# Kernel tuning notes

Measured on AMD Instinct MI355X. Metric: run time of the kernel, lower is better.

## Reference

```python
import jax, jax.numpy as jnp
import numpy as np

N_ENT = 40000      # n_ent_vocab
NUM_POS = 24       # n_rel_vocab // 2
N_REL = 48         # n_rel_vocab (fwd + inverse relations)
BODY_LEN = 3
N_EDGES = 300000
BATCH = 64
THR = 1e-20


def setup_inputs() -> dict:
    key = jax.random.key(0)
    ks = jax.random.split(key, 8)
    return {
        "q_head": jax.random.randint(ks[0], (BATCH,), 0, N_ENT, dtype=jnp.int32),
        "q_rel": jax.random.randint(ks[1], (BATCH,), 0, NUM_POS, dtype=jnp.int32),
        "t": jax.random.randint(ks[2], (BATCH,), 0, N_ENT, dtype=jnp.int32),
        # dec_output is a softmax over relations -> positive weights in (0,1)
        "attention": jax.random.uniform(ks[3], (BATCH, BODY_LEN, N_REL), dtype=jnp.float32),
        "edge_head": jax.random.randint(ks[4], (N_EDGES,), 0, N_ENT, dtype=jnp.int32),
        "edge_tail": jax.random.randint(ks[5], (N_EDGES,), 0, N_ENT, dtype=jnp.int32),
        "edge_rel": jax.random.randint(ks[6], (N_EDGES,), 0, NUM_POS, dtype=jnp.int32),
        # uncertain-KG confidence values stored in the sparse adjacency
        "edge_val": jax.random.uniform(ks[7], (N_EDGES,), dtype=jnp.float32),
    }


def reference(q_head, q_rel, t, attention, edge_head, edge_tail, edge_rel, edge_val):
    """Fused equivalent of Translator.forwardAllNLP.

    database[r] are sparse [N_ENT, N_ENT] matrices; here the whole multigraph is
    one edge list (edge_head, edge_tail, edge_rel, edge_val). torch.sparse.mm
    per relation + attention-weighted accumulation becomes a single gather /
    segment_sum pass over all relations at once.
    """
    B = q_head.shape[0]
    # zero out the query triples in the (shared) database, as in the torch code
    killed = ((edge_head[None, :] == q_head[:, None])
              & (edge_tail[None, :] == t[:, None])
              & (edge_rel[None, :] == q_rel[:, None])).any(axis=0)
    vals = jnp.where(killed, 0.0, edge_val)  # [E]

    mem = jax.nn.one_hot(q_head, N_ENT, dtype=jnp.float32)  # [B, N_ENT]
    for step in range(BODY_LEN):
        attn = attention[:, step]                 # [B, N_REL]
        a_fwd = attn[:, edge_rel]                 # [B, E]  attention[:,step,r]
        a_rev = attn[:, edge_rel + NUM_POS]       # [B, E]  attention[:,step,r+num_pos]
        gh = mem[:, edge_head] * vals             # [B, E]  sparse.mm(mem, A_r)
        gt = mem[:, edge_tail] * vals             # [B, E]  sparse.mm(mem, A_r^T)
        fwd_msg = jax.ops.segment_sum((gh * a_fwd).T, edge_tail, num_segments=N_ENT).T
        rev_msg = jax.ops.segment_sum((gt * a_rev).T, edge_head, num_segments=N_ENT).T
        # self-loop term: memories * attention[:, step, -1]
        mem = fwd_msg + rev_msg + mem * attn[:, -1:]

    mem = mem / jnp.maximum(THR, mem.sum(axis=1, keepdims=True))
    # -sum(one_hot(t) * log(max(thr, mem))) == -log(max(thr, mem[b, t[b]]))
    tgt_prob = mem[jnp.arange(B), t]
    batch_loss = -jnp.log(jnp.maximum(THR, tgt_prob)).mean()
    return batch_loss, mem
```

## Files before the change

### kernel.cpp

```cpp
#include <hip/hip_runtime.h>

#define N_ENT 40000
#define NB 64
#define BODY_LEN 3
#define N_REL 48
#define NUM_POS 24
#define THR 1e-20f

#define NBK 157
#define PA_BLOCKS 320
#define DEC_BLOCKS 320
#define FLIST_LDS 192


__global__ void k_zero(int* __restrict__ bktCnt, int* __restrict__ fcnt,
                       float* __restrict__ sums) {
    int t = threadIdx.x;
    if (t < NBK) bktCnt[t] = 0;
    if (t < 3) fcnt[t] = 0;
    if (t < NB) sums[t] = 0.0f;
}

__global__ void k_bhist(const int* __restrict__ eh, const int* __restrict__ et,
                        int* __restrict__ bktCnt, int nE) {
    __shared__ int h[NBK];
    int tid = threadIdx.x;
    for (int i = tid; i < NBK; i += 256) h[i] = 0;
    __syncthreads();
    for (int i = blockIdx.x * 256 + tid; i < nE; i += gridDim.x * 256) {
        atomicAdd(&h[eh[i] >> 8], 1);
        atomicAdd(&h[et[i] >> 8], 1);
    }
    __syncthreads();
    for (int i = tid; i < NBK; i += 256)
        if (h[i]) atomicAdd(&bktCnt[i], h[i]);
}

__global__ void k_bscan(const int* __restrict__ bktCnt, int* __restrict__ bktBase,
                        int* __restrict__ bktCur, int* __restrict__ offs) {
    __shared__ int s[256];
    int t = threadIdx.x;
    int v = (t < NBK) ? bktCnt[t] : 0;
    s[t] = v;
    __syncthreads();
    for (int off = 1; off < 256; off <<= 1) {
        int add = (t >= off) ? s[t - off] : 0;
        __syncthreads();
        s[t] += add;
        __syncthreads();
    }
    if (t < NBK) {
        int ex = s[t] - v;
        bktBase[t] = ex;
        bktCur[t] = ex;
    }
    if (t == NBK - 1) {
        bktBase[NBK] = s[t];
        offs[N_ENT] = s[t];
    }
}

__global__ void k_passA(const int* __restrict__ qh, const int* __restrict__ qr,
                        const int* __restrict__ tq, const int* __restrict__ eh,
                        const int* __restrict__ et, const int* __restrict__ er,
                        const float* __restrict__ ev, int* __restrict__ bktCur,
                        uint2* __restrict__ items, int nE) {
    __shared__ long long s_key[NB];
    __shared__ int h[NBK];
    __shared__ int myB[NBK];
    int tid = threadIdx.x;
    if (tid < NB)
        s_key[tid] = ((long long)qh[tid] << 32) | ((long long)tq[tid] << 8) | (long long)qr[tid];
    for (int i = tid; i < NBK; i += 256) h[i] = 0;
    __syncthreads();
    int chunk = (nE + PA_BLOCKS - 1) / PA_BLOCKS;
    int b0 = blockIdx.x * chunk;
    int b1 = min(nE, b0 + chunk);
    for (int i = b0 + tid; i < b1; i += 256) {
        atomicAdd(&h[eh[i] >> 8], 1);
        atomicAdd(&h[et[i] >> 8], 1);
    }
    __syncthreads();
    for (int i = tid; i < NBK; i += 256) {
        int c = h[i];
        myB[i] = c ? atomicAdd(&bktCur[i], c) : 0;
        h[i] = 0;
    }
    __syncthreads();
    for (int i = b0 + tid; i < b1; i += 256) {
        int hh = eh[i], te = et[i], r = er[i];
        long long k = ((long long)hh << 32) | ((long long)te << 8) | (long long)r;
        bool killed = false;
#pragma unroll
        for (int b = 0; b < NB; ++b) killed |= (s_key[b] == k);
        unsigned vb = killed ? 0u : __float_as_uint(ev[i]);
        int bk1 = hh >> 8;
        int rk1 = atomicAdd(&h[bk1], 1);
        items[myB[bk1] + rk1] =
            make_uint2((unsigned)te | ((unsigned)r << 16) | ((unsigned)(hh & 255) << 24), vb);
        int bk2 = te >> 8;
        int rk2 = atomicAdd(&h[bk2], 1);
        items[myB[bk2] + rk2] =
            make_uint2((unsigned)hh | ((unsigned)(r + NUM_POS) << 16) | ((unsigned)(te & 255) << 24), vb);
    }
}

__global__ void k_passB(const uint2* __restrict__ itemsA, const int* __restrict__ bktBase,
                        int* __restrict__ offs, uint2* __restrict__ csr) {
    __shared__ int cnt[256];
    __shared__ int sc[256];
    int tid = threadIdx.x;
    int b = blockIdx.x;
    int e0 = b << 8;
    int eCnt = min(256, N_ENT - e0);
    cnt[tid] = 0;
    __syncthreads();
    int ib = bktBase[b];
    int n = bktBase[b + 1] - ib;
    for (int i = tid; i < n; i += 256)
        atomicAdd(&cnt[itemsA[ib + i].x >> 24], 1);
    __syncthreads();
    int v = cnt[tid];
    sc[tid] = v;
    __syncthreads();
    for (int off = 1; off < 256; off <<= 1) {
        int add = (tid >= off) ? sc[tid - off] : 0;
        __syncthreads();
        sc[tid] += add;
        __syncthreads();
    }
    int ex = sc[tid] - v;
    if (tid < eCnt) offs[e0 + tid] = ib + ex;
    cnt[tid] = ex;
    __syncthreads();
    for (int i = tid; i < n; i += 256) {
        uint2 it = itemsA[ib + i];
        int k = (int)(it.x >> 24);
        int p = atomicAdd(&cnt[k], 1);
        csr[ib + p] = it;
    }
}

__device__ __forceinline__ void flag_entities(unsigned long long m, int lane,
                                              int ent, int* s_cnt, int* s_list) {
    bool flag = ((lane & 15) == 0) && ((m >> lane) & 0xFFFFULL);
    unsigned long long am = __ballot(flag);
    if (am) {
        int leader = __ffsll((long long)am) - 1;
        int lb = 0;
        if (lane == leader) lb = atomicAdd(s_cnt, __popcll(am));
        lb = __shfl(lb, leader);
        if (flag) {
            int rank = __popcll(am & ((1ULL << lane) - 1ULL));
            s_list[lb + rank] = ent;
        }
    }
}

__global__ void k_init_decay(const int* __restrict__ qh, const float* __restrict__ attn,
                             float* __restrict__ nxt, int* __restrict__ fcnt,
                             int* __restrict__ flist) {
    __shared__ float s_d[NB];
    __shared__ int s_q[NB];
    __shared__ int s_list[FLIST_LDS];
    __shared__ int s_cnt, s_gbase;
    int tid = threadIdx.x;
    if (tid < NB) {
        s_d[tid] = attn[tid * (BODY_LEN * N_REL) + 0 * N_REL + (N_REL - 1)];
        s_q[tid] = qh[tid];
    }
    if (tid == 0) s_cnt = 0;
    __syncthreads();
    int lane = tid & 63;
    const int total4 = NB * N_ENT / 4;
    for (int i4 = blockIdx.x * 256 + tid; i4 < total4; i4 += gridDim.x * 256) {
        int ent = (i4 * 4) >> 6;
        int b0 = (i4 * 4) & 63;
        float4 w;
        w.x = (s_q[b0 + 0] == ent) ? s_d[b0 + 0] : 0.0f;
        w.y = (s_q[b0 + 1] == ent) ? s_d[b0 + 1] : 0.0f;
        w.z = (s_q[b0 + 2] == ent) ? s_d[b0 + 2] : 0.0f;
        w.w = (s_q[b0 + 3] == ent) ? s_d[b0 + 3] : 0.0f;
        ((float4*)nxt)[i4] = w;
        bool nz = (s_q[b0 + 0] == ent) | (s_q[b0 + 1] == ent) |
                  (s_q[b0 + 2] == ent) | (s_q[b0 + 3] == ent);
        unsigned long long m = __ballot(nz);
        flag_entities(m, lane, ent, &s_cnt, s_list);
    }
    __syncthreads();
    if (tid == 0 && s_cnt) s_gbase = atomicAdd(fcnt, s_cnt);
    __syncthreads();
    for (int i = tid; i < s_cnt; i += 256) flist[s_gbase + i] = s_list[i];
}

__global__ void k_decay(const float* __restrict__ oldm, float* __restrict__ nxt,
                        const float* __restrict__ attn, int step,
                        int* __restrict__ fcnt, int* __restrict__ flist) {
    __shared__ float s_d[NB];
    __shared__ int s_list[FLIST_LDS];
    __shared__ int s_cnt, s_gbase;
    int tid = threadIdx.x;
    if (tid < NB)
        s_d[tid] = attn[tid * (BODY_LEN * N_REL) + step * N_REL + (N_REL - 1)];
    if (tid == 0) s_cnt = 0;
    __syncthreads();
    int lane = tid & 63;
    const int total4 = NB * N_ENT / 4;
    for (int i4 = blockIdx.x * 256 + tid; i4 < total4; i4 += gridDim.x * 256) {
        float4 v = ((const float4*)oldm)[i4];
        int b0 = (tid * 4) & 63;
        float4 w;
        w.x = v.x * s_d[b0 + 0];
        w.y = v.y * s_d[b0 + 1];
        w.z = v.z * s_d[b0 + 2];
        w.w = v.w * s_d[b0 + 3];
        ((float4*)nxt)[i4] = w;
        bool nz = (v.x != 0.0f) | (v.y != 0.0f) | (v.z != 0.0f) | (v.w != 0.0f);
        unsigned long long m = __ballot(nz);
        flag_entities(m, lane, (i4 * 4) >> 6, &s_cnt, s_list);
    }
    __syncthreads();
    if (tid == 0 && s_cnt) s_gbase = atomicAdd(fcnt, s_cnt);
    __syncthreads();
    for (int i = tid; i < s_cnt; i += 256) flist[s_gbase + i] = s_list[i];
}

template <bool STEP0>
__global__ __launch_bounds__(256) void k_fstep(
    const uint2* __restrict__ csr, const int* __restrict__ offs,
    const int* __restrict__ flist, const int* __restrict__ fcnt,
    const float* __restrict__ attn, int step,
    const float* __restrict__ oldm, const int* __restrict__ qh,
    float* __restrict__ nxt) {
    __shared__ float s_attn[NB][N_REL + 1];
    int tid = threadIdx.x;
    for (int idx = tid; idx < NB * N_REL; idx += 256) {
        int b = idx / N_REL, r = idx % N_REL;
        s_attn[b][r] = attn[b * (BODY_LEN * N_REL) + step * N_REL + r];
    }
    __syncthreads();
    int lane = tid & 63;
    int myqh = STEP0 ? qh[lane] : 0;
    int n = *fcnt;
    int w = (blockIdx.x * 256 + tid) >> 6;
    int nW = (gridDim.x * 256) >> 6;
    for (int f = w; f < n; f += nW) {
        int e = flist[f];
        float src = STEP0 ? ((myqh == e) ? 1.0f : 0.0f)
                          : oldm[(size_t)e * 64 + lane];
        int base = offs[e];
        int cnt = offs[e + 1] - base;
        for (int k0 = 0; k0 < cnt; k0 += 64) {
            uint2 slot = make_uint2(0u, 0u);
            if (k0 + lane < cnt) slot = csr[base + k0 + lane];
            int lim = min(64, cnt - k0);
            for (int j = 0; j < lim; ++j) {
                unsigned meta = (unsigned)__shfl((int)slot.x, j);
                float v = __uint_as_float((unsigned)__shfl((int)slot.y, j));
                if (v == 0.0f) continue;
                float val = src * v * s_attn[lane][(meta >> 16) & 63];
                if (val != 0.0f)
                    atomicAdd(&nxt[(size_t)(meta & 0xFFFFu) * 64 + lane], val);
            }
        }
    }
}

__global__ void k_sums(const float* __restrict__ mem, float* __restrict__ sums) {
    __shared__ float s_s[NB];
    if (threadIdx.x < NB) s_s[threadIdx.x] = 0.0f;
    __syncthreads();
    const float4* m4 = (const float4*)mem;
    const int total4 = NB * N_ENT / 4;
    float4 acc = {0.0f, 0.0f, 0.0f, 0.0f};
    for (int i = blockIdx.x * 256 + threadIdx.x; i < total4; i += gridDim.x * 256) {
        float4 v = m4[i];
        acc.x += v.x; acc.y += v.y; acc.z += v.z; acc.w += v.w;
    }
    int b0 = (threadIdx.x * 4) & 63;
    atomicAdd(&s_s[b0 + 0], acc.x);
    atomicAdd(&s_s[b0 + 1], acc.y);
    atomicAdd(&s_s[b0 + 2], acc.z);
    atomicAdd(&s_s[b0 + 3], acc.w);
    __syncthreads();
    if (threadIdx.x < NB) atomicAdd(&sums[threadIdx.x], s_s[threadIdx.x]);
}

__global__ void k_norm_tr(const float* __restrict__ mem, const float* __restrict__ sums,
                          const int* __restrict__ tt, float* __restrict__ out) {
    if (blockIdx.x == N_ENT / 64) {
        int b = threadIdx.x;
        if (b < 64) {
            float p = mem[(size_t)tt[b] * 64 + b] / fmaxf(THR, sums[b]);
            float l = -logf(fmaxf(THR, p));
#pragma unroll
            for (int off = 32; off > 0; off >>= 1) l += __shfl_down(l, off);
            if (b == 0) out[0] = l * (1.0f / 64.0f);
        }
        return;
    }
    __shared__ float tile[64][65];
    __shared__ float s_inv[64];
    int tid = threadIdx.x;
    int e0 = blockIdx.x * 64;
    if (tid < 64) s_inv[tid] = 1.0f / fmaxf(THR, sums[tid]);
    const float4* m4 = (const float4*)(mem + (size_t)e0 * 64);
#pragma unroll
    for (int k = 0; k < 4; ++k) {
        int i4 = k * 256 + tid;
        float4 v = m4[i4];
        int el = i4 >> 4, b0 = (i4 * 4) & 63;
        tile[el][b0 + 0] = v.x; tile[el][b0 + 1] = v.y;
        tile[el][b0 + 2] = v.z; tile[el][b0 + 3] = v.w;
    }
    __syncthreads();
#pragma unroll
    for (int k = 0; k < 16; ++k) {
        int idx = k * 256 + tid;
        int el = idx & 63, b = idx >> 6;
        out[1 + (size_t)b * N_ENT + e0 + el] = tile[el][b] * s_inv[b];
    }
}

extern "C" void kernel_launch(void* const* d_in, const int* in_sizes, int n_in,
                              void* d_out, int out_size, void* d_ws, size_t ws_size,
                              hipStream_t stream) {
    const int*   qh   = (const int*)d_in[0];
    const int*   qr   = (const int*)d_in[1];
    const int*   tt   = (const int*)d_in[2];
    const float* attn = (const float*)d_in[3];
    const int*   eh   = (const int*)d_in[4];
    const int*   et   = (const int*)d_in[5];
    const int*   er   = (const int*)d_in[6];
    const float* ev   = (const float*)d_in[7];
    float* out = (float*)d_out;
    int nE = in_sizes[4];

    const size_t MEM_BYTES = (size_t)NB * N_ENT * sizeof(float);
    char* ws = (char*)d_ws;
    int*   offs    = (int*)ws;
    int*   flist   = (int*)(ws + (192u << 10));
    int*   bktCnt  = (int*)(ws + (384u << 10));
    int*   bktBase = (int*)(ws + (388u << 10));
    int*   bktCur  = (int*)(ws + (392u << 10));
    int*   fcnt    = (int*)(ws + (396u << 10));
    float* sums    = (float*)(ws + (400u << 10));
    uint2* csr     = (uint2*)(ws + (1u << 20));
    float* memA    = (float*)(ws + (6u << 20));
    float* memB;
    uint2* itemsA;
    size_t itemsBytes = (size_t)2 * nE * sizeof(uint2);
    size_t needBoth = (size_t)(6u << 20) + 2 * MEM_BYTES + itemsBytes;
    if (ws_size >= needBoth) {
        memB   = (float*)(ws + (6u << 20) + MEM_BYTES);
        itemsA = (uint2*)(ws + (6u << 20) + 2 * MEM_BYTES);
    } else {
        memB   = out + 1;
        itemsA = (uint2*)(out + 1);
    }

    k_zero<<<1, 256, 0, stream>>>(bktCnt, fcnt, sums);
    k_bhist<<<PA_BLOCKS, 256, 0, stream>>>(eh, et, bktCnt, nE);
    k_bscan<<<1, 256, 0, stream>>>(bktCnt, bktBase, bktCur, offs);
    k_passA<<<PA_BLOCKS, 256, 0, stream>>>(qh, qr, tt, eh, et, er, ev, bktCur, itemsA, nE);
    k_passB<<<NBK, 256, 0, stream>>>(itemsA, bktBase, offs, csr);

    k_init_decay<<<DEC_BLOCKS, 256, 0, stream>>>(qh, attn, memA, fcnt + 0, flist);
    k_fstep<true><<<16, 256, 0, stream>>>(csr, offs, flist, fcnt + 0, attn, 0,
                                          nullptr, qh, memA);
    float* curm = memA;
    float* nxtm = memB;
    for (int s = 1; s < BODY_LEN; ++s) {
        k_decay<<<DEC_BLOCKS, 256, 0, stream>>>(curm, nxtm, attn, s, fcnt + s, flist);
        k_fstep<false><<<1024, 256, 0, stream>>>(csr, offs, flist, fcnt + s, attn, s,
                                                 curm, nullptr, nxtm);
        float* tmp = curm; curm = nxtm; nxtm = tmp;
    }

    k_sums<<<128, 256, 0, stream>>>(curm, sums);
    k_norm_tr<<<N_ENT / 64 + 1, 256, 0, stream>>>(curm, sums, tt, out);
}
```

Before: 200.1 us.

## Switch propagation to pull-based gather with per-entity activity flags

```diff
diff --git a/kernel.cpp b/kernel.cpp
--- a/kernel.cpp
+++ b/kernel.cpp
@@ -9,39 +9,36 @@
 
 #define NBK 157
 #define PA_BLOCKS 320
-#define DEC_BLOCKS 320
-#define FLIST_LDS 192
-
-
-__global__ void k_zero(int* __restrict__ bktCnt, int* __restrict__ fcnt,
-                       float* __restrict__ sums) {
-    int t = threadIdx.x;
-    if (t < NBK) bktCnt[t] = 0;
-    if (t < 3) fcnt[t] = 0;
-    if (t < NB) sums[t] = 0.0f;
-}
-
-__global__ void k_bhist(const int* __restrict__ eh, const int* __restrict__ et,
-                        int* __restrict__ bktCnt, int nE) {
+#define STEP_BLOCKS 2048
+
+
+__global__ void k_hist(const int* __restrict__ eh, const int* __restrict__ et,
+                       int* __restrict__ pHist, int nE) {
     __shared__ int h[NBK];
     int tid = threadIdx.x;
     for (int i = tid; i < NBK; i += 256) h[i] = 0;
     __syncthreads();
-    for (int i = blockIdx.x * 256 + tid; i < nE; i += gridDim.x * 256) {
+    int chunk = (nE + PA_BLOCKS - 1) / PA_BLOCKS;
+    int b0 = blockIdx.x * chunk, b1 = min(nE, b0 + chunk);
+    for (int i = b0 + tid; i < b1; i += 256) {
+        atomicAdd(&h[et[i] >> 8], 1);
         atomicAdd(&h[eh[i] >> 8], 1);
-        atomicAdd(&h[et[i] >> 8], 1);
-    }
-    __syncthreads();
-    for (int i = tid; i < NBK; i += 256)
-        if (h[i]) atomicAdd(&bktCnt[i], h[i]);
-}
-
-__global__ void k_bscan(const int* __restrict__ bktCnt, int* __restrict__ bktBase,
-                        int* __restrict__ bktCur, int* __restrict__ offs) {
+    }
+    __syncthreads();
+    for (int i = tid; i < NBK; i += 256) pHist[blockIdx.x * NBK + i] = h[i];
+}
+
+__global__ void k_bscan(int* __restrict__ pHist, int* __restrict__ bktBase,
+                        int* __restrict__ offs, const int* __restrict__ qh,
+                        unsigned char* __restrict__ act0, float* __restrict__ sums) {
     __shared__ int s[256];
     int t = threadIdx.x;
-    int v = (t < NBK) ? bktCnt[t] : 0;
-    s[t] = v;
+    int tot = 0;
+    if (t < NBK) {
+#pragma unroll 8
+        for (int i = 0; i < PA_BLOCKS; ++i) tot += pHist[i * NBK + t];
+    }
+    s[t] = tot;
     __syncthreads();
     for (int off = 1; off < 256; off <<= 1) {
         int add = (t >= off) ? s[t - off] : 0;
@@ -49,44 +46,38 @@
         s[t] += add;
         __syncthreads();
     }
+    int ex = s[t] - tot;
+    if (t < NBK) bktBase[t] = ex;
+    if (t == NBK - 1) { bktBase[NBK] = s[t]; offs[N_ENT] = s[t]; }
     if (t < NBK) {
-        int ex = s[t] - v;
-        bktBase[t] = ex;
-        bktCur[t] = ex;
-    }
-    if (t == NBK - 1) {
-        bktBase[NBK] = s[t];
-        offs[N_ENT] = s[t];
-    }
+        int run = ex;
+#pragma unroll 4
+        for (int i = 0; i < PA_BLOCKS; ++i) {
+            int c = pHist[i * NBK + t];
+            pHist[i * NBK + t] = run;
+            run += c;
+        }
+    }
+    for (int i = t; i < N_ENT; i += 256) act0[i] = 0;
+    for (int i = t; i < NB * 16; i += 256) sums[i] = 0.0f;
+    __syncthreads();
+    if (t < NB) act0[qh[t]] = 1;
 }
 
 __global__ void k_passA(const int* __restrict__ qh, const int* __restrict__ qr,
                         const int* __restrict__ tq, const int* __restrict__ eh,
                         const int* __restrict__ et, const int* __restrict__ er,
-                        const float* __restrict__ ev, int* __restrict__ bktCur,
+                        const float* __restrict__ ev, const int* __restrict__ pBase,
                         uint2* __restrict__ items, int nE) {
     __shared__ long long s_key[NB];
-    __shared__ int h[NBK];
-    __shared__ int myB[NBK];
+    __shared__ int cur[NBK];
     int tid = threadIdx.x;
     if (tid < NB)
         s_key[tid] = ((long long)qh[tid] << 32) | ((long long)tq[tid] << 8) | (long long)qr[tid];
-    for (int i = tid; i < NBK; i += 256) h[i] = 0;
+    for (int i = tid; i < NBK; i += 256) cur[i] = pBase[blockIdx.x * NBK + i];
     __syncthreads();
     int chunk = (nE + PA_BLOCKS - 1) / PA_BLOCKS;
-    int b0 = blockIdx.x * chunk;
-    int b1 = min(nE, b0 + chunk);
-    for (int i = b0 + tid; i < b1; i += 256) {
-        atomicAdd(&h[eh[i] >> 8], 1);
-        atomicAdd(&h[et[i] >> 8], 1);
-    }
-    __syncthreads();
-    for (int i = tid; i < NBK; i += 256) {
-        int c = h[i];
-        myB[i] = c ? atomicAdd(&bktCur[i], c) : 0;
-        h[i] = 0;
-    }
-    __syncthreads();
+    int b0 = blockIdx.x * chunk, b1 = min(nE, b0 + chunk);
     for (int i = b0 + tid; i < b1; i += 256) {
         int hh = eh[i], te = et[i], r = er[i];
         long long k = ((long long)hh << 32) | ((long long)te << 8) | (long long)r;
@@ -94,14 +85,14 @@
 #pragma unroll
         for (int b = 0; b < NB; ++b) killed |= (s_key[b] == k);
         unsigned vb = killed ? 0u : __float_as_uint(ev[i]);
-        int bk1 = hh >> 8;
-        int rk1 = atomicAdd(&h[bk1], 1);
-        items[myB[bk1] + rk1] =
-            make_uint2((unsigned)te | ((unsigned)r << 16) | ((unsigned)(hh & 255) << 24), vb);
-        int bk2 = te >> 8;
-        int rk2 = atomicAdd(&h[bk2], 1);
-        items[myB[bk2] + rk2] =
-            make_uint2((unsigned)hh | ((unsigned)(r + NUM_POS) << 16) | ((unsigned)(te & 255) << 24), vb);
+        int bk = te >> 8;
+        int p = atomicAdd(&cur[bk], 1);
+        items[p] = make_uint2((unsigned)hh | ((unsigned)r << 16) |
+                              ((unsigned)(te & 255) << 24), vb);
+        bk = hh >> 8;
+        p = atomicAdd(&cur[bk], 1);
+        items[p] = make_uint2((unsigned)te | ((unsigned)(r + NUM_POS) << 16) |
+                              ((unsigned)(hh & 255) << 24), vb);
     }
 }
 
@@ -141,149 +132,68 @@
     }
 }
 
-__device__ __forceinline__ void flag_entities(unsigned long long m, int lane,
-                                              int ent, int* s_cnt, int* s_list) {
-    bool flag = ((lane & 15) == 0) && ((m >> lane) & 0xFFFFULL);
-    unsigned long long am = __ballot(flag);
-    if (am) {
-        int leader = __ffsll((long long)am) - 1;
-        int lb = 0;
-        if (lane == leader) lb = atomicAdd(s_cnt, __popcll(am));
-        lb = __shfl(lb, leader);
-        if (flag) {
-            int rank = __popcll(am & ((1ULL << lane) - 1ULL));
-            s_list[lb + rank] = ent;
-        }
-    }
-}
-
-__global__ void k_init_decay(const int* __restrict__ qh, const float* __restrict__ attn,
-                             float* __restrict__ nxt, int* __restrict__ fcnt,
-                             int* __restrict__ flist) {
-    __shared__ float s_d[NB];
+template <int STEP>
+__global__ __launch_bounds__(256) void k_step(
+    const uint2* __restrict__ csr, const int* __restrict__ offs,
+    const unsigned char* __restrict__ actIn, unsigned char* __restrict__ actOut,
+    const float* __restrict__ attn, const float* __restrict__ oldm,
+    const int* __restrict__ qh, float* __restrict__ nxt, float* __restrict__ sums) {
+    __shared__ float s_attn[NB][N_REL + 1];
+    __shared__ float s_dlast[NB];
     __shared__ int s_q[NB];
-    __shared__ int s_list[FLIST_LDS];
-    __shared__ int s_cnt, s_gbase;
-    int tid = threadIdx.x;
-    if (tid < NB) {
-        s_d[tid] = attn[tid * (BODY_LEN * N_REL) + 0 * N_REL + (N_REL - 1)];
-        s_q[tid] = qh[tid];
-    }
-    if (tid == 0) s_cnt = 0;
-    __syncthreads();
-    int lane = tid & 63;
-    const int total4 = NB * N_ENT / 4;
-    for (int i4 = blockIdx.x * 256 + tid; i4 < total4; i4 += gridDim.x * 256) {
-        int ent = (i4 * 4) >> 6;
-        int b0 = (i4 * 4) & 63;
-        float4 w;
-        w.x = (s_q[b0 + 0] == ent) ? s_d[b0 + 0] : 0.0f;
-        w.y = (s_q[b0 + 1] == ent) ? s_d[b0 + 1] : 0.0f;
-        w.z = (s_q[b0 + 2] == ent) ? s_d[b0 + 2] : 0.0f;
-        w.w = (s_q[b0 + 3] == ent) ? s_d[b0 + 3] : 0.0f;
-        ((float4*)nxt)[i4] = w;
-        bool nz = (s_q[b0 + 0] == ent) | (s_q[b0 + 1] == ent) |
-                  (s_q[b0 + 2] == ent) | (s_q[b0 + 3] == ent);
-        unsigned long long m = __ballot(nz);
-        flag_entities(m, lane, ent, &s_cnt, s_list);
-    }
-    __syncthreads();
-    if (tid == 0 && s_cnt) s_gbase = atomicAdd(fcnt, s_cnt);
-    __syncthreads();
-    for (int i = tid; i < s_cnt; i += 256) flist[s_gbase + i] = s_list[i];
-}
-
-__global__ void k_decay(const float* __restrict__ oldm, float* __restrict__ nxt,
-                        const float* __restrict__ attn, int step,
-                        int* __restrict__ fcnt, int* __restrict__ flist) {
-    __shared__ float s_d[NB];
-    __shared__ int s_list[FLIST_LDS];
-    __shared__ int s_cnt, s_gbase;
-    int tid = threadIdx.x;
-    if (tid < NB)
-        s_d[tid] = attn[tid * (BODY_LEN * N_REL) + step * N_REL + (N_REL - 1)];
-    if (tid == 0) s_cnt = 0;
-    __syncthreads();
-    int lane = tid & 63;
-    const int total4 = NB * N_ENT / 4;
-    for (int i4 = blockIdx.x * 256 + tid; i4 < total4; i4 += gridDim.x * 256) {
-        float4 v = ((const float4*)oldm)[i4];
-        int b0 = (tid * 4) & 63;
-        float4 w;
-        w.x = v.x * s_d[b0 + 0];
-        w.y = v.y * s_d[b0 + 1];
-        w.z = v.z * s_d[b0 + 2];
-        w.w = v.w * s_d[b0 + 3];
-        ((float4*)nxt)[i4] = w;
-        bool nz = (v.x != 0.0f) | (v.y != 0.0f) | (v.z != 0.0f) | (v.w != 0.0f);
-        unsigned long long m = __ballot(nz);
-        flag_entities(m, lane, (i4 * 4) >> 6, &s_cnt, s_list);
-    }
-    __syncthreads();
-    if (tid == 0 && s_cnt) s_gbase = atomicAdd(fcnt, s_cnt);
-    __syncthreads();
-    for (int i = tid; i < s_cnt; i += 256) flist[s_gbase + i] = s_list[i];
-}
-
-template <bool STEP0>
-__global__ __launch_bounds__(256) void k_fstep(
-    const uint2* __restrict__ csr, const int* __restrict__ offs,
-    const int* __restrict__ flist, const int* __restrict__ fcnt,
-    const float* __restrict__ attn, int step,
-    const float* __restrict__ oldm, const int* __restrict__ qh,
-    float* __restrict__ nxt) {
-    __shared__ float s_attn[NB][N_REL + 1];
-    int tid = threadIdx.x;
+    __shared__ float s_s[NB];
+    int tid = threadIdx.x, lane = tid & 63;
     for (int idx = tid; idx < NB * N_REL; idx += 256) {
         int b = idx / N_REL, r = idx % N_REL;
-        s_attn[b][r] = attn[b * (BODY_LEN * N_REL) + step * N_REL + r];
-    }
-    __syncthreads();
-    int lane = tid & 63;
-    int myqh = STEP0 ? qh[lane] : 0;
-    int n = *fcnt;
+        s_attn[b][r] = attn[b * (BODY_LEN * N_REL) + STEP * N_REL + r];
+    }
+    if (tid < NB) {
+        s_dlast[tid] = attn[tid * (BODY_LEN * N_REL) + STEP * N_REL + (N_REL - 1)];
+        if (STEP == 0) s_q[tid] = qh[tid];
+        if (STEP == 2) s_s[tid] = 0.0f;
+    }
+    __syncthreads();
+    int myq = (STEP == 0) ? s_q[lane] : 0;
+    float colsum = 0.0f;
     int w = (blockIdx.x * 256 + tid) >> 6;
     int nW = (gridDim.x * 256) >> 6;
-    for (int f = w; f < n; f += nW) {
-        int e = flist[f];
-        float src = STEP0 ? ((myqh == e) ? 1.0f : 0.0f)
-                          : oldm[(size_t)e * 64 + lane];
-        int base = offs[e];
-        int cnt = offs[e + 1] - base;
+    for (int d = w; d < N_ENT; d += nW) {
+        float acc = 0.0f;
+        if (STEP == 0) {
+            acc = (myq == d) ? s_dlast[lane] : 0.0f;
+        } else {
+            if (actIn[d]) acc = oldm[(size_t)d * 64 + lane] * s_dlast[lane];
+        }
+        int base = offs[d];
+        int cnt = offs[d + 1] - base;
         for (int k0 = 0; k0 < cnt; k0 += 64) {
-            uint2 slot = make_uint2(0u, 0u);
-            if (k0 + lane < cnt) slot = csr[base + k0 + lane];
-            int lim = min(64, cnt - k0);
-            for (int j = 0; j < lim; ++j) {
-                unsigned meta = (unsigned)__shfl((int)slot.x, j);
-                float v = __uint_as_float((unsigned)__shfl((int)slot.y, j));
-                if (v == 0.0f) continue;
-                float val = src * v * s_attn[lane][(meta >> 16) & 63];
-                if (val != 0.0f)
-                    atomicAdd(&nxt[(size_t)(meta & 0xFFFFu) * 64 + lane], val);
+            int i = k0 + lane;
+            uint2 it = (i < cnt) ? csr[base + i] : make_uint2(0u, 0u);
+            bool on = (i < cnt) && (it.y != 0u) && actIn[it.x & 0xFFFFu];
+            unsigned long long m = __ballot(on);
+            while (m) {
+                int j = __ffsll((long long)m) - 1;
+                m &= m - 1;
+                unsigned mx = (unsigned)__shfl((int)it.x, j);
+                float v = __uint_as_float((unsigned)__shfl((int)it.y, j));
+                int s2 = (int)(mx & 0xFFFFu);
+                float sv = (STEP == 0) ? ((myq == s2) ? 1.0f : 0.0f)
+                                       : oldm[(size_t)s2 * 64 + lane];
+                acc += sv * v * s_attn[lane][(mx >> 16) & 63];
             }
         }
-    }
-}
-
-__global__ void k_sums(const float* __restrict__ mem, float* __restrict__ sums) {
-    __shared__ float s_s[NB];
-    if (threadIdx.x < NB) s_s[threadIdx.x] = 0.0f;
-    __syncthreads();
-    const float4* m4 = (const float4*)mem;
-    const int total4 = NB * N_ENT / 4;
-    float4 acc = {0.0f, 0.0f, 0.0f, 0.0f};
-    for (int i = blockIdx.x * 256 + threadIdx.x; i < total4; i += gridDim.x * 256) {
-        float4 v = m4[i];
-        acc.x += v.x; acc.y += v.y; acc.z += v.z; acc.w += v.w;
-    }
-    int b0 = (threadIdx.x * 4) & 63;
-    atomicAdd(&s_s[b0 + 0], acc.x);
-    atomicAdd(&s_s[b0 + 1], acc.y);
-    atomicAdd(&s_s[b0 + 2], acc.z);
-    atomicAdd(&s_s[b0 + 3], acc.w);
-    __syncthreads();
-    if (threadIdx.x < NB) atomicAdd(&sums[threadIdx.x], s_s[threadIdx.x]);
+        nxt[(size_t)d * 64 + lane] = acc;
+        if (STEP < 2) {
+            unsigned long long nz = __ballot(acc != 0.0f);
+            if (lane == 0) actOut[d] = nz ? 1 : 0;
+        }
+        if (STEP == 2) colsum += acc;
+    }
+    if (STEP == 2) {
+        atomicAdd(&s_s[lane], colsum);
+        __syncthreads();
+        if (tid < NB) atomicAdd(&sums[tid * 16], s_s[tid]);
+    }
 }
 
 __global__ void k_norm_tr(const float* __restrict__ mem, const float* __restrict__ sums,
@@ -291,7 +201,7 @@
     if (blockIdx.x == N_ENT / 64) {
         int b = threadIdx.x;
         if (b < 64) {
-            float p = mem[(size_t)tt[b] * 64 + b] / fmaxf(THR, sums[b]);
+            float p = mem[(size_t)tt[b] * 64 + b] / fmaxf(THR, sums[b * 16]);
             float l = -logf(fmaxf(THR, p));
 #pragma unroll
             for (int off = 32; off > 0; off >>= 1) l += __shfl_down(l, off);
@@ -303,7 +213,7 @@
     __shared__ float s_inv[64];
     int tid = threadIdx.x;
     int e0 = blockIdx.x * 64;
-    if (tid < 64) s_inv[tid] = 1.0f / fmaxf(THR, sums[tid]);
+    if (tid < 64) s_inv[tid] = 1.0f / fmaxf(THR, sums[tid * 16]);
     const float4* m4 = (const float4*)(mem + (size_t)e0 * 64);
 #pragma unroll
     for (int k = 0; k < 4; ++k) {
@@ -339,12 +249,11 @@
     const size_t MEM_BYTES = (size_t)NB * N_ENT * sizeof(float);
     char* ws = (char*)d_ws;
     int*   offs    = (int*)ws;
-    int*   flist   = (int*)(ws + (192u << 10));
-    int*   bktCnt  = (int*)(ws + (384u << 10));
-    int*   bktBase = (int*)(ws + (388u << 10));
-    int*   bktCur  = (int*)(ws + (392u << 10));
-    int*   fcnt    = (int*)(ws + (396u << 10));
-    float* sums    = (float*)(ws + (400u << 10));
+    int*   bktBase = (int*)(ws + (192u << 10));
+    int*   pHist   = (int*)(ws + (196u << 10));
+    unsigned char* act0 = (unsigned char*)(ws + (452u << 10));
+    unsigned char* act1 = (unsigned char*)(ws + (512u << 10));
+    float* sums    = (float*)(ws + (576u << 10));
     uint2* csr     = (uint2*)(ws + (1u << 20));
     float* memA    = (float*)(ws + (6u << 20));
     float* memB;
@@ -359,24 +268,17 @@
         itemsA = (uint2*)(out + 1);
     }
 
-    k_zero<<<1, 256, 0, stream>>>(bktCnt, fcnt, sums);
-    k_bhist<<<PA_BLOCKS, 256, 0, stream>>>(eh, et, bktCnt, nE);
-    k_bscan<<<1, 256, 0, stream>>>(bktCnt, bktBase, bktCur, offs);
-    k_passA<<<PA_BLOCKS, 256, 0, stream>>>(qh, qr, tt, eh, et, er, ev, bktCur, itemsA, nE);
+    k_hist<<<PA_BLOCKS, 256, 0, stream>>>(eh, et, pHist, nE);
+    k_bscan<<<1, 256, 0, stream>>>(pHist, bktBase, offs, qh, act0, sums);
+    k_passA<<<PA_BLOCKS, 256, 0, stream>>>(qh, qr, tt, eh, et, er, ev, pHist, itemsA, nE);
     k_passB<<<NBK, 256, 0, stream>>>(itemsA, bktBase, offs, csr);
 
-    k_init_decay<<<DEC_BLOCKS, 256, 0, stream>>>(qh, attn, memA, fcnt + 0, flist);
-    k_fstep<true><<<16, 256, 0, stream>>>(csr, offs, flist, fcnt + 0, attn, 0,
-                                          nullptr, qh, memA);
-    float* curm = memA;
-    float* nxtm = memB;
-    for (int s = 1; s < BODY_LEN; ++s) {
-        k_decay<<<DEC_BLOCKS, 256, 0, stream>>>(curm, nxtm, attn, s, fcnt + s, flist);
-        k_fstep<false><<<1024, 256, 0, stream>>>(csr, offs, flist, fcnt + s, attn, s,
-                                                 curm, nullptr, nxtm);
-        float* tmp = curm; curm = nxtm; nxtm = tmp;
-    }
-
-    k_sums<<<128, 256, 0, stream>>>(curm, sums);
-    k_norm_tr<<<N_ENT / 64 + 1, 256, 0, stream>>>(curm, sums, tt, out);
-}
+    k_step<0><<<STEP_BLOCKS, 256, 0, stream>>>(csr, offs, act0, act1, attn,
+                                               nullptr, qh, memA, nullptr);
+    k_step<1><<<STEP_BLOCKS, 256, 0, stream>>>(csr, offs, act1, act0, attn,
+                                               memA, qh, memB, nullptr);
+    k_step<2><<<STEP_BLOCKS, 256, 0, stream>>>(csr, offs, act0, nullptr, attn,
+                                               memB, qh, memA, sums);
+
+    k_norm_tr<<<N_ENT / 64 + 1, 256, 0, stream>>>(memA, sums, tt, out);
+}
```

Result: slower. 232.2 us (+16.0%).

## Fuse setup kernels, use per-block histogram offsets, fold column sums into final step

Applied to the files above, without the earlier changes.

```diff
diff --git a/kernel.cpp b/kernel.cpp
--- a/kernel.cpp
+++ b/kernel.cpp
@@ -7,86 +7,115 @@
 #define NUM_POS 24
 #define THR 1e-20f
 
-#define NBK 157
+#define NBK 313
 #define PA_BLOCKS 320
 #define DEC_BLOCKS 320
 #define FLIST_LDS 192
 
 
-__global__ void k_zero(int* __restrict__ bktCnt, int* __restrict__ fcnt,
-                       float* __restrict__ sums) {
+__global__ void k_build0(const int* __restrict__ eh, const int* __restrict__ et,
+                         int* __restrict__ pHist, const int* __restrict__ qh,
+                         const float* __restrict__ attn, float* __restrict__ memA,
+                         int* __restrict__ fcnt, int* __restrict__ flist,
+                         float* __restrict__ sums, int nE) {
+    int tid = threadIdx.x;
+    if (blockIdx.x < PA_BLOCKS) {
+        __shared__ int h[NBK];
+        for (int i = tid; i < NBK; i += 256) h[i] = 0;
+        __syncthreads();
+        int chunk = (nE + PA_BLOCKS - 1) / PA_BLOCKS;
+        int b0 = blockIdx.x * chunk, b1 = min(nE, b0 + chunk);
+        for (int i = b0 + tid; i < b1; i += 256) {
+            atomicAdd(&h[eh[i] >> 7], 1);
+            atomicAdd(&h[et[i] >> 7], 1);
+        }
+        __syncthreads();
+        for (int i = tid; i < NBK; i += 256) pHist[blockIdx.x * NBK + i] = h[i];
+    } else {
+        __shared__ float s_d[NB];
+        __shared__ int s_q[NB];
+        if (tid < NB) {
+            s_d[tid] = attn[tid * (BODY_LEN * N_REL) + 0 * N_REL + (N_REL - 1)];
+            s_q[tid] = qh[tid];
+        }
+        __syncthreads();
+        int ib = blockIdx.x - PA_BLOCKS;
+        const int total4 = NB * N_ENT / 4;
+        for (int i4 = ib * 256 + tid; i4 < total4; i4 += 320 * 256) {
+            int ent = (i4 * 4) >> 6;
+            int b0 = (i4 * 4) & 63;
+            float4 w;
+            w.x = (s_q[b0 + 0] == ent) ? s_d[b0 + 0] : 0.0f;
+            w.y = (s_q[b0 + 1] == ent) ? s_d[b0 + 1] : 0.0f;
+            w.z = (s_q[b0 + 2] == ent) ? s_d[b0 + 2] : 0.0f;
+            w.w = (s_q[b0 + 3] == ent) ? s_d[b0 + 3] : 0.0f;
+            ((float4*)memA)[i4] = w;
+        }
+        if (ib == 0) {
+            for (int i = tid; i < NB * 16; i += 256) sums[i] = 0.0f;
+            if (tid < 64) {
+                int q = s_q[tid];
+                bool first = true;
+                for (int j = 0; j < tid; ++j) first &= (s_q[j] != q);
+                unsigned long long mf = __ballot(first);
+                int pos = __popcll(mf & ((1ULL << tid) - 1ULL));
+                if (first) flist[pos] = q;
+                if (tid == 0) fcnt[0] = __popcll(mf);
+                if (tid == 1) fcnt[1] = 0;
+                if (tid == 2) fcnt[2] = 0;
+            }
+        }
+    }
+}
+
+__global__ void k_bcol(int* __restrict__ pHist, int* __restrict__ bktTot) {
+    __shared__ int s[512];
+    int t = threadIdx.x, b = blockIdx.x;
+    int v = (t < PA_BLOCKS) ? pHist[t * NBK + b] : 0;
+    s[t] = v;
+    __syncthreads();
+    for (int off = 1; off < 512; off <<= 1) {
+        int add = (t >= off) ? s[t - off] : 0;
+        __syncthreads();
+        s[t] += add;
+        __syncthreads();
+    }
+    if (t < PA_BLOCKS) pHist[t * NBK + b] = s[t] - v;
+    if (t == PA_BLOCKS - 1) bktTot[b] = s[t];
+}
+
+__global__ void k_bscan_small(const int* __restrict__ bktTot, int* __restrict__ bktBase,
+                              int* __restrict__ offs) {
+    __shared__ int s[512];
     int t = threadIdx.x;
-    if (t < NBK) bktCnt[t] = 0;
-    if (t < 3) fcnt[t] = 0;
-    if (t < NB) sums[t] = 0.0f;
-}
-
-__global__ void k_bhist(const int* __restrict__ eh, const int* __restrict__ et,
-                        int* __restrict__ bktCnt, int nE) {
-    __shared__ int h[NBK];
-    int tid = threadIdx.x;
-    for (int i = tid; i < NBK; i += 256) h[i] = 0;
-    __syncthreads();
-    for (int i = blockIdx.x * 256 + tid; i < nE; i += gridDim.x * 256) {
-        atomicAdd(&h[eh[i] >> 8], 1);
-        atomicAdd(&h[et[i] >> 8], 1);
-    }
-    __syncthreads();
-    for (int i = tid; i < NBK; i += 256)
-        if (h[i]) atomicAdd(&bktCnt[i], h[i]);
-}
-
-__global__ void k_bscan(const int* __restrict__ bktCnt, int* __restrict__ bktBase,
-                        int* __restrict__ bktCur, int* __restrict__ offs) {
-    __shared__ int s[256];
-    int t = threadIdx.x;
-    int v = (t < NBK) ? bktCnt[t] : 0;
+    int v = (t < NBK) ? bktTot[t] : 0;
     s[t] = v;
     __syncthreads();
-    for (int off = 1; off < 256; off <<= 1) {
+    for (int off = 1; off < 512; off <<= 1) {
         int add = (t >= off) ? s[t - off] : 0;
         __syncthreads();
         s[t] += add;
         __syncthreads();
     }
-    if (t < NBK) {
-        int ex = s[t] - v;
-        bktBase[t] = ex;
-        bktCur[t] = ex;
-    }
-    if (t == NBK - 1) {
-        bktBase[NBK] = s[t];
-        offs[N_ENT] = s[t];
-    }
+    if (t < NBK) bktBase[t] = s[t] - v;
+    if (t == NBK - 1) { bktBase[NBK] = s[t]; offs[N_ENT] = s[t]; }
 }
 
 __global__ void k_passA(const int* __restrict__ qh, const int* __restrict__ qr,
                         const int* __restrict__ tq, const int* __restrict__ eh,
                         const int* __restrict__ et, const int* __restrict__ er,
-                        const float* __restrict__ ev, int* __restrict__ bktCur,
-                        uint2* __restrict__ items, int nE) {
+                        const float* __restrict__ ev, const int* __restrict__ pBase,
+                        const int* __restrict__ bktBase, uint2* __restrict__ items, int nE) {
     __shared__ long long s_key[NB];
-    __shared__ int h[NBK];
-    __shared__ int myB[NBK];
+    __shared__ int cur[NBK];
     int tid = threadIdx.x;
     if (tid < NB)
         s_key[tid] = ((long long)qh[tid] << 32) | ((long long)tq[tid] << 8) | (long long)qr[tid];
-    for (int i = tid; i < NBK; i += 256) h[i] = 0;
+    for (int i = tid; i < NBK; i += 256)
+        cur[i] = bktBase[i] + pBase[blockIdx.x * NBK + i];
     __syncthreads();
     int chunk = (nE + PA_BLOCKS - 1) / PA_BLOCKS;
-    int b0 = blockIdx.x * chunk;
-    int b1 = min(nE, b0 + chunk);
-    for (int i = b0 + tid; i < b1; i += 256) {
-        atomicAdd(&h[eh[i] >> 8], 1);
-        atomicAdd(&h[et[i] >> 8], 1);
-    }
-    __syncthreads();
-    for (int i = tid; i < NBK; i += 256) {
-        int c = h[i];
-        myB[i] = c ? atomicAdd(&bktCur[i], c) : 0;
-        h[i] = 0;
-    }
-    __syncthreads();
+    int b0 = blockIdx.x * chunk, b1 = min(nE, b0 + chunk);
     for (int i = b0 + tid; i < b1; i += 256) {
         int hh = eh[i], te = et[i], r = er[i];
         long long k = ((long long)hh << 32) | ((long long)te << 8) | (long long)r;
@@ -94,33 +123,33 @@
 #pragma unroll
         for (int b = 0; b < NB; ++b) killed |= (s_key[b] == k);
         unsigned vb = killed ? 0u : __float_as_uint(ev[i]);
-        int bk1 = hh >> 8;
-        int rk1 = atomicAdd(&h[bk1], 1);
-        items[myB[bk1] + rk1] =
-            make_uint2((unsigned)te | ((unsigned)r << 16) | ((unsigned)(hh & 255) << 24), vb);
-        int bk2 = te >> 8;
-        int rk2 = atomicAdd(&h[bk2], 1);
-        items[myB[bk2] + rk2] =
-            make_uint2((unsigned)hh | ((unsigned)(r + NUM_POS) << 16) | ((unsigned)(te & 255) << 24), vb);
+        int bk = hh >> 7;
+        int p = atomicAdd(&cur[bk], 1);
+        items[p] = make_uint2((unsigned)te | ((unsigned)r << 16) |
+                              ((unsigned)(hh & 127) << 24), vb);
+        bk = te >> 7;
+        p = atomicAdd(&cur[bk], 1);
+        items[p] = make_uint2((unsigned)hh | ((unsigned)(r + NUM_POS) << 16) |
+                              ((unsigned)(te & 127) << 24), vb);
     }
 }
 
 __global__ void k_passB(const uint2* __restrict__ itemsA, const int* __restrict__ bktBase,
                         int* __restrict__ offs, uint2* __restrict__ csr) {
-    __shared__ int cnt[256];
+    __shared__ int cnt[128];
     __shared__ int sc[256];
     int tid = threadIdx.x;
     int b = blockIdx.x;
-    int e0 = b << 8;
-    int eCnt = min(256, N_ENT - e0);
-    cnt[tid] = 0;
+    int e0 = b << 7;
+    int eCnt = min(128, N_ENT - e0);
+    if (tid < 128) cnt[tid] = 0;
     __syncthreads();
     int ib = bktBase[b];
     int n = bktBase[b + 1] - ib;
     for (int i = tid; i < n; i += 256)
         atomicAdd(&cnt[itemsA[ib + i].x >> 24], 1);
     __syncthreads();
-    int v = cnt[tid];
+    int v = (tid < 128) ? cnt[tid] : 0;
     sc[tid] = v;
     __syncthreads();
     for (int off = 1; off < 256; off <<= 1) {
@@ -131,7 +160,7 @@
     }
     int ex = sc[tid] - v;
     if (tid < eCnt) offs[e0 + tid] = ib + ex;
-    cnt[tid] = ex;
+    if (tid < 128) cnt[tid] = ex;
     __syncthreads();
     for (int i = tid; i < n; i += 256) {
         uint2 it = itemsA[ib + i];
@@ -157,64 +186,34 @@
     }
 }
 
-__global__ void k_init_decay(const int* __restrict__ qh, const float* __restrict__ attn,
-                             float* __restrict__ nxt, int* __restrict__ fcnt,
-                             int* __restrict__ flist) {
+__global__ void k_decay(const float* __restrict__ oldm, float* __restrict__ nxt,
+                        const float* __restrict__ attn, int step,
+                        int* __restrict__ fcnt, int* __restrict__ flist,
+                        float* __restrict__ sums) {
     __shared__ float s_d[NB];
-    __shared__ int s_q[NB];
+    __shared__ float s_s[NB];
     __shared__ int s_list[FLIST_LDS];
     __shared__ int s_cnt, s_gbase;
     int tid = threadIdx.x;
     if (tid < NB) {
-        s_d[tid] = attn[tid * (BODY_LEN * N_REL) + 0 * N_REL + (N_REL - 1)];
-        s_q[tid] = qh[tid];
+        s_d[tid] = attn[tid * (BODY_LEN * N_REL) + step * N_REL + (N_REL - 1)];
+        s_s[tid] = 0.0f;
     }
     if (tid == 0) s_cnt = 0;
     __syncthreads();
     int lane = tid & 63;
-    const int total4 = NB * N_ENT / 4;
-    for (int i4 = blockIdx.x * 256 + tid; i4 < total4; i4 += gridDim.x * 256) {
-        int ent = (i4 * 4) >> 6;
-        int b0 = (i4 * 4) & 63;
-        float4 w;
-        w.x = (s_q[b0 + 0] == ent) ? s_d[b0 + 0] : 0.0f;
-        w.y = (s_q[b0 + 1] == ent) ? s_d[b0 + 1] : 0.0f;
-        w.z = (s_q[b0 + 2] == ent) ? s_d[b0 + 2] : 0.0f;
-        w.w = (s_q[b0 + 3] == ent) ? s_d[b0 + 3] : 0.0f;
-        ((float4*)nxt)[i4] = w;
-        bool nz = (s_q[b0 + 0] == ent) | (s_q[b0 + 1] == ent) |
-                  (s_q[b0 + 2] == ent) | (s_q[b0 + 3] == ent);
-        unsigned long long m = __ballot(nz);
-        flag_entities(m, lane, ent, &s_cnt, s_list);
-    }
-    __syncthreads();
-    if (tid == 0 && s_cnt) s_gbase = atomicAdd(fcnt, s_cnt);
-    __syncthreads();
-    for (int i = tid; i < s_cnt; i += 256) flist[s_gbase + i] = s_list[i];
-}
-
-__global__ void k_decay(const float* __restrict__ oldm, float* __restrict__ nxt,
-                        const float* __restrict__ attn, int step,
-                        int* __restrict__ fcnt, int* __restrict__ flist) {
-    __shared__ float s_d[NB];
-    __shared__ int s_list[FLIST_LDS];
-    __shared__ int s_cnt, s_gbase;
-    int tid = threadIdx.x;
-    if (tid < NB)
-        s_d[tid] = attn[tid * (BODY_LEN * N_REL) + step * N_REL + (N_REL - 1)];
-    if (tid == 0) s_cnt = 0;
-    __syncthreads();
-    int lane = tid & 63;
+    int b0 = (tid * 4) & 63;
+    float cs0 = 0.0f, cs1 = 0.0f, cs2 = 0.0f, cs3 = 0.0f;
     const int total4 = NB * N_ENT / 4;
     for (int i4 = blockIdx.x * 256 + tid; i4 < total4; i4 += gridDim.x * 256) {
         float4 v = ((const float4*)oldm)[i4];
-        int b0 = (tid * 4) & 63;
         float4 w;
         w.x = v.x * s_d[b0 + 0];
         w.y = v.y * s_d[b0 + 1];
         w.z = v.z * s_d[b0 + 2];
         w.w = v.w * s_d[b0 + 3];
         ((float4*)nxt)[i4] = w;
+        if (sums) { cs0 += w.x; cs1 += w.y; cs2 += w.z; cs3 += w.w; }
         bool nz = (v.x != 0.0f) | (v.y != 0.0f) | (v.z != 0.0f) | (v.w != 0.0f);
         unsigned long long m = __ballot(nz);
         flag_entities(m, lane, (i4 * 4) >> 6, &s_cnt, s_list);
@@ -223,6 +222,14 @@
     if (tid == 0 && s_cnt) s_gbase = atomicAdd(fcnt, s_cnt);
     __syncthreads();
     for (int i = tid; i < s_cnt; i += 256) flist[s_gbase + i] = s_list[i];
+    if (sums) {
+        atomicAdd(&s_s[b0 + 0], cs0);
+        atomicAdd(&s_s[b0 + 1], cs1);
+        atomicAdd(&s_s[b0 + 2], cs2);
+        atomicAdd(&s_s[b0 + 3], cs3);
+        __syncthreads();
+        if (tid < NB) atomicAdd(&sums[tid * 16], s_s[tid]);
+    }
 }
 
 template <bool STEP0>
@@ -231,16 +238,19 @@
     const int* __restrict__ flist, const int* __restrict__ fcnt,
     const float* __restrict__ attn, int step,
     const float* __restrict__ oldm, const int* __restrict__ qh,
-    float* __restrict__ nxt) {
+    float* __restrict__ nxt, float* __restrict__ sums) {
     __shared__ float s_attn[NB][N_REL + 1];
+    __shared__ float s_s[NB];
     int tid = threadIdx.x;
     for (int idx = tid; idx < NB * N_REL; idx += 256) {
         int b = idx / N_REL, r = idx % N_REL;
         s_attn[b][r] = attn[b * (BODY_LEN * N_REL) + step * N_REL + r];
     }
+    if (tid < NB) s_s[tid] = 0.0f;
     __syncthreads();
     int lane = tid & 63;
     int myqh = STEP0 ? qh[lane] : 0;
+    float colsum = 0.0f;
     int n = *fcnt;
     int w = (blockIdx.x * 256 + tid) >> 6;
     int nW = (gridDim.x * 256) >> 6;
@@ -259,31 +269,18 @@
                 float v = __uint_as_float((unsigned)__shfl((int)slot.y, j));
                 if (v == 0.0f) continue;
                 float val = src * v * s_attn[lane][(meta >> 16) & 63];
-                if (val != 0.0f)
+                if (val != 0.0f) {
                     atomicAdd(&nxt[(size_t)(meta & 0xFFFFu) * 64 + lane], val);
+                    if (sums) colsum += val;
+                }
             }
         }
     }
-}
-
-__global__ void k_sums(const float* __restrict__ mem, float* __restrict__ sums) {
-    __shared__ float s_s[NB];
-    if (threadIdx.x < NB) s_s[threadIdx.x] = 0.0f;
-    __syncthreads();
-    const float4* m4 = (const float4*)mem;
-    const int total4 = NB * N_ENT / 4;
-    float4 acc = {0.0f, 0.0f, 0.0f, 0.0f};
-    for (int i = blockIdx.x * 256 + threadIdx.x; i < total4; i += gridDim.x * 256) {
-        float4 v = m4[i];
-        acc.x += v.x; acc.y += v.y; acc.z += v.z; acc.w += v.w;
-    }
-    int b0 = (threadIdx.x * 4) & 63;
-    atomicAdd(&s_s[b0 + 0], acc.x);
-    atomicAdd(&s_s[b0 + 1], acc.y);
-    atomicAdd(&s_s[b0 + 2], acc.z);
-    atomicAdd(&s_s[b0 + 3], acc.w);
-    __syncthreads();
-    if (threadIdx.x < NB) atomicAdd(&sums[threadIdx.x], s_s[threadIdx.x]);
+    if (sums) {
+        atomicAdd(&s_s[lane], colsum);
+        __syncthreads();
+        if (tid < NB) atomicAdd(&sums[tid * 16], s_s[tid]);
+    }
 }
 
 __global__ void k_norm_tr(const float* __restrict__ mem, const float* __restrict__ sums,
@@ -291,7 +288,7 @@
     if (blockIdx.x == N_ENT / 64) {
         int b = threadIdx.x;
         if (b < 64) {
-            float p = mem[(size_t)tt[b] * 64 + b] / fmaxf(THR, sums[b]);
+            float p = mem[(size_t)tt[b] * 64 + b] / fmaxf(THR, sums[b * 16]);
             float l = -logf(fmaxf(THR, p));
 #pragma unroll
             for (int off = 32; off > 0; off >>= 1) l += __shfl_down(l, off);
@@ -303,7 +300,7 @@
     __shared__ float s_inv[64];
     int tid = threadIdx.x;
     int e0 = blockIdx.x * 64;
-    if (tid < 64) s_inv[tid] = 1.0f / fmaxf(THR, sums[tid]);
+    if (tid < 64) s_inv[tid] = 1.0f / fmaxf(THR, sums[tid * 16]);
     const float4* m4 = (const float4*)(mem + (size_t)e0 * 64);
 #pragma unroll
     for (int k = 0; k < 4; ++k) {
@@ -340,11 +337,11 @@
     char* ws = (char*)d_ws;
     int*   offs    = (int*)ws;
     int*   flist   = (int*)(ws + (192u << 10));
-    int*   bktCnt  = (int*)(ws + (384u << 10));
-    int*   bktBase = (int*)(ws + (388u << 10));
-    int*   bktCur  = (int*)(ws + (392u << 10));
-    int*   fcnt    = (int*)(ws + (396u << 10));
-    float* sums    = (float*)(ws + (400u << 10));
+    int*   pHist   = (int*)(ws + (384u << 10));
+    int*   bktTot  = (int*)(ws + (896u << 10));
+    int*   bktBase = (int*)(ws + (900u << 10));
+    int*   fcnt    = (int*)(ws + (904u << 10));
+    float* sums    = (float*)(ws + (908u << 10));
     uint2* csr     = (uint2*)(ws + (1u << 20));
     float* memA    = (float*)(ws + (6u << 20));
     float* memB;
@@ -359,24 +356,22 @@
         itemsA = (uint2*)(out + 1);
     }
 
-    k_zero<<<1, 256, 0, stream>>>(bktCnt, fcnt, sums);
-    k_bhist<<<PA_BLOCKS, 256, 0, stream>>>(eh, et, bktCnt, nE);
-    k_bscan<<<1, 256, 0, stream>>>(bktCnt, bktBase, bktCur, offs);
-    k_passA<<<PA_BLOCKS, 256, 0, stream>>>(qh, qr, tt, eh, et, er, ev, bktCur, itemsA, nE);
+    k_build0<<<2 * PA_BLOCKS, 256, 0, stream>>>(eh, et, pHist, qh, attn, memA,
+                                                fcnt, flist, sums, nE);
+    k_bcol<<<NBK, 512, 0, stream>>>(pHist, bktTot);
+    k_bscan_small<<<1, 512, 0, stream>>>(bktTot, bktBase, offs);
+    k_passA<<<PA_BLOCKS, 256, 0, stream>>>(qh, qr, tt, eh, et, er, ev, pHist,
+                                           bktBase, itemsA, nE);
     k_passB<<<NBK, 256, 0, stream>>>(itemsA, bktBase, offs, csr);
 
-    k_init_decay<<<DEC_BLOCKS, 256, 0, stream>>>(qh, attn, memA, fcnt + 0, flist);
     k_fstep<true><<<16, 256, 0, stream>>>(csr, offs, flist, fcnt + 0, attn, 0,
-                                          nullptr, qh, memA);
-    float* curm = memA;
-    float* nxtm = memB;
-    for (int s = 1; s < BODY_LEN; ++s) {
-        k_decay<<<DEC_BLOCKS, 256, 0, stream>>>(curm, nxtm, attn, s, fcnt + s, flist);
-        k_fstep<false><<<1024, 256, 0, stream>>>(csr, offs, flist, fcnt + s, attn, s,
-                                                 curm, nullptr, nxtm);
-        float* tmp = curm; curm = nxtm; nxtm = tmp;
-    }
-
-    k_sums<<<128, 256, 0, stream>>>(curm, sums);
-    k_norm_tr<<<N_ENT / 64 + 1, 256, 0, stream>>>(curm, sums, tt, out);
-}
+                                          nullptr, qh, memA, nullptr);
+    k_decay<<<DEC_BLOCKS, 256, 0, stream>>>(memA, memB, attn, 1, fcnt + 1, flist, nullptr);
+    k_fstep<false><<<1024, 256, 0, stream>>>(csr, offs, flist, fcnt + 1, attn, 1,
+                                             memA, nullptr, memB, nullptr);
+    k_decay<<<DEC_BLOCKS, 256, 0, stream>>>(memB, memA, attn, 2, fcnt + 2, flist, sums);
+    k_fstep<false><<<1024, 256, 0, stream>>>(csr, offs, flist, fcnt + 2, attn, 2,
+                                             memB, nullptr, memA, sums);
+
+    k_norm_tr<<<N_ENT / 64 + 1, 256, 0, stream>>>(memA, sums, tt, out);
+}
```

After: 210.0 us. +4.9%, slower.
